# Performance work log

Hardware: AMD Instinct MI355X
Metric: run time of the kernel (lower is better)

## Reference

```python
import jax, jax.numpy as jnp
import numpy as np

B = 1
HEIGHT, WIDTH = 30, 52
HW = HEIGHT * WIDTH            # 1560
TQ = 2                         # query blocks -> Qtot = 3120
TK = 8                         # history blocks -> Ktot = 12480
KPQ = 2                        # selected kv blocks per query block
QTOT = TQ * HW
KTOT = TK * HW
HEADS = 12
DH = 128
DIM = HEADS * DH               # 1536, inner_dim == dim
EPS = 1e-5


def _rope_tables(S, D):
    # interleaved RoPE tables: freqs_cos[..., 0::2] == cos(ang), freqs_sin[..., 1::2] == sin(ang)
    inv_freq = 1.0 / (10000.0 ** (np.arange(0, D, 2, dtype=np.float32) / D))
    ang = np.arange(S, dtype=np.float32)[:, None] * inv_freq[None, :]      # [S, D/2]
    cos = np.repeat(np.cos(ang), 2, axis=-1)                                # [S, D]
    sin = np.repeat(np.sin(ang), 2, axis=-1)
    return (jnp.asarray(cos)[None, :, None, :], jnp.asarray(sin)[None, :, None, :])


def setup_inputs() -> dict:
    key = jax.random.key(0)
    ks = jax.random.split(key, 12)
    hidden_states = jax.random.normal(ks[0], (B, QTOT, DIM), jnp.float32)
    history_states = jax.random.normal(ks[1], (B, KTOT, DIM), jnp.float32)
    freqs_cos, freqs_sin = _rope_tables(QTOT, DH)
    freqs_cos_his, freqs_sin_his = _rope_tables(KTOT, DH)
    # first selected block always valid, second may be -1 (masked)
    sel0 = jax.random.randint(ks[2], (B, TQ, 1), 0, TK)
    sel1 = jax.random.randint(ks[3], (B, TQ, 1), -1, TK)
    sel_k_blocks = jnp.concatenate([sel0, sel1], axis=-1).astype(jnp.int32)  # [B, TQ, KPQ]
    s = 0.02
    Wq = jax.random.normal(ks[4], (DIM, DIM), jnp.float32) * s
    Wk = jax.random.normal(ks[5], (DIM, DIM), jnp.float32) * s
    Wv = jax.random.normal(ks[6], (DIM, DIM), jnp.float32) * s
    Wo = jax.random.normal(ks[7], (DIM, DIM), jnp.float32) * s
    bq = jnp.zeros((DIM,), jnp.float32)
    bk = jnp.zeros((DIM,), jnp.float32)
    bv = jnp.zeros((DIM,), jnp.float32)
    bo = jnp.zeros((DIM,), jnp.float32)
    gq = jnp.ones((DIM,), jnp.float32)
    gk = jnp.ones((DIM,), jnp.float32)
    return dict(hidden_states=hidden_states, history_states=history_states,
                freqs_cos=freqs_cos, freqs_sin=freqs_sin,
                freqs_cos_his=freqs_cos_his, freqs_sin_his=freqs_sin_his,
                sel_k_blocks=sel_k_blocks,
                Wq=Wq, bq=bq, Wk=Wk, bk=bk, Wv=Wv, bv=bv, Wo=Wo, bo=bo, gq=gq, gk=gk)


def _rmsnorm(x, g):
    return x * jax.lax.rsqrt(jnp.mean(x * x, axis=-1, keepdims=True) + EPS) * g


def _apply_rope(x, fc, fs):
    # x: [B, S, H, D]; fc/fs: [1, S, 1, D] interleaved tables
    x1 = x[..., 0::2]
    x2 = x[..., 1::2]
    cos = fc[..., 0::2]
    sin = fs[..., 1::2]
    even = x1 * cos - x2 * sin
    odd = x1 * sin + x2 * cos
    return jnp.stack([even, odd], axis=-1).reshape(x.shape)


def reference(hidden_states, history_states, freqs_cos, freqs_sin,
              freqs_cos_his, freqs_sin_his, sel_k_blocks,
              Wq, bq, Wk, bk, Wv, bv, Wo, bo, gq, gk):
    Bn, Qtot, _ = hidden_states.shape
    # projections + RMSNorm
    q = _rmsnorm(hidden_states @ Wq.T + bq, gq)
    k = _rmsnorm(history_states @ Wk.T + bk, gk)
    v = history_states @ Wv.T + bv
    q = q.reshape(Bn, QTOT, HEADS, DH)
    k = k.reshape(Bn, KTOT, HEADS, DH)
    v = v.reshape(Bn, KTOT, HEADS, DH)
    q = _apply_rope(q, freqs_cos, freqs_sin)
    k = _apply_rope(k, freqs_cos_his, freqs_sin_his)
    # [B, Hh, S, D] then blocked
    q_blk = q.transpose(0, 2, 1, 3).reshape(Bn, HEADS, TQ, HW, DH)
    k_blk = k.transpose(0, 2, 1, 3).reshape(Bn, HEADS, TK, HW, DH)
    v_blk = v.transpose(0, 2, 1, 3).reshape(Bn, HEADS, TK, HW, DH)
    # gather selected kv blocks (clamped indices; invalid masked later)
    idx = jnp.clip(sel_k_blocks, 0).reshape(Bn, TQ * KPQ)          # [B, TQ*KPQ]
    gather = jax.vmap(lambda kb, ib: kb[:, ib])                     # over batch
    k_sel = gather(k_blk, idx).reshape(Bn, HEADS, TQ, KPQ * HW, DH)
    v_sel = gather(v_blk, idx).reshape(Bn, HEADS, TQ, KPQ * HW, DH)
    scale = 1.0 / jnp.sqrt(jnp.float32(DH))
    scores = jnp.einsum('bhtqd,bhtkd->bhtqk', q_blk, k_sel) * scale  # [B,Hh,TQ,HW,KPQ*HW]
    valid = (sel_k_blocks >= 0)                                      # [B,TQ,KPQ]
    mask = jnp.repeat(valid, HW, axis=-1)[:, None, :, None, :]       # [B,1,TQ,1,KPQ*HW]
    scores = jnp.where(mask, scores, -jnp.inf)
    attnw = jax.nn.softmax(scores, axis=-1)
    out = jnp.einsum('bhtqk,bhtkd->bhtqd', attnw, v_sel)             # [B,Hh,TQ,HW,DH]
    out = out.reshape(Bn, HEADS, QTOT, DH).transpose(0, 2, 1, 3).reshape(Bn, QTOT, HEADS * DH)
    return out @ Wo.T + bo
```

## Files before the change

kernel.cpp:

```cpp
#include <hip/hip_runtime.h>

typedef unsigned short u16;
typedef __attribute__((ext_vector_type(4))) unsigned short u16x4;
typedef __attribute__((ext_vector_type(8))) unsigned short u16x8;
typedef __attribute__((ext_vector_type(4))) short s16x4;
typedef __attribute__((ext_vector_type(4))) float f32x4;
typedef __attribute__((ext_vector_type(8))) __bf16 bf16x8;

__device__ __forceinline__ u16 f2bf(float f) {
  union { float f; unsigned int u; } v; v.f = f;
  unsigned int u = v.u;
  unsigned int r = (u + 0x7fffu + ((u >> 16) & 1u)) >> 16;
  return (u16)r;
}
__device__ __forceinline__ u16 f2bf_hw(float f) {
  return __builtin_bit_cast(u16, (__bf16)f);
}
__device__ __forceinline__ float bf2f(u16 h) {
  union { unsigned int u; float f; } v; v.u = ((unsigned int)h) << 16;
  return v.f;
}
__device__ __forceinline__ f32x4 mfma16(u16x8 a, u16x8 b, f32x4 c) {
  return __builtin_amdgcn_mfma_f32_16x16x32_bf16(
      __builtin_bit_cast(bf16x8, a), __builtin_bit_cast(bf16x8, b), c, 0, 0, 0);
}
__device__ __forceinline__ f32x4 mfma16k16(u16x4 a, u16x4 b, f32x4 c) {
  return __builtin_amdgcn_mfma_f32_16x16x16bf16_1k(
      __builtin_bit_cast(s16x4, a), __builtin_bit_cast(s16x4, b), c, 0, 0, 0);
}
__device__ __forceinline__ void glds16(const void* g, void* l) {
  __builtin_amdgcn_global_load_lds((const __attribute__((address_space(1))) void*)g,
                                   (__attribute__((address_space(3))) void*)l, 16, 0, 0);
}
__device__ __forceinline__ int xcd_chunk(int bid, int nwg) {
  int xcd = bid & 7, idx = bid >> 3;
  int q = nwg >> 3, r = nwg & 7;
  int base = xcd < r ? xcd * (q + 1) : r * (q + 1) + (xcd - r) * q;
  return base + idx;
}
__device__ __forceinline__ int sel_mask(const int* __restrict__ sel) {
  int m = 0;
#pragma unroll
  for (int tt = 0; tt < 2; ++tt) {
    int a = sel[2 * tt];
    if (a < 0) a = 0;
    m |= 1 << a;
    int b = sel[2 * tt + 1];
    if (b >= 0) m |= 1 << b;
  }
  return m;
}

__global__ __launch_bounds__(256) void cvt_all(
    const float* __restrict__ hs, const float* __restrict__ his,
    const float* __restrict__ Wq, const float* __restrict__ Wk,
    const float* __restrict__ Wv, const float* __restrict__ Wo,
    u16* __restrict__ hsb, u16* __restrict__ hib,
    u16* __restrict__ wqb, u16* __restrict__ wkb,
    u16* __restrict__ wvb, u16* __restrict__ wob) {
  const int N0 = 1198080, N1 = 5990400, N2 = 6580224, N3 = 7170048, N4 = 7759872;
  int i = blockIdx.x * 256 + threadIdx.x;
  const float* s; u16* o; int base;
  if (i < N0)      { s = hs;  o = hsb; base = 0;  }
  else if (i < N1) { s = his; o = hib; base = N0; }
  else if (i < N2) { s = Wq;  o = wqb; base = N1; }
  else if (i < N3) { s = Wk;  o = wkb; base = N2; }
  else if (i < N4) { s = Wv;  o = wvb; base = N3; }
  else             { s = Wo;  o = wob; base = N4; }
  int j = i - base;
  float4 v = ((const float4*)s)[j];
  u16x4 r;
  r.x = f2bf(v.x); r.y = f2bf(v.y); r.z = f2bf(v.z); r.w = f2bf(v.w);
  ((u16x4*)o)[j] = r;
}

template <int OUT, int NBX>
__global__ __launch_bounds__(256, 2) void gemm_v2(
    const u16* __restrict__ A, const u16* __restrict__ W,
    const float* __restrict__ bias, void* __restrict__ Cp, int M) {
  const int K = 1536, N = 1536;
  __shared__ __align__(16) u16 gsm[17408];
  u16* As = gsm;
  u16* Bs = gsm + 8192;
  const int tid = threadIdx.x;
  const int lane = tid & 63, wid = tid >> 6;
  const int quad = lane >> 4, l15 = lane & 15;
  const int lg = xcd_chunk(blockIdx.x, gridDim.x);
  const int m0 = (lg / NBX) * 128, n0 = (lg % NBX) * 128;
  const int wm = (wid >> 1) * 64, wn = (wid & 1) * 64;
  f32x4 acc[4][4];
#pragma unroll
  for (int i = 0; i < 4; ++i)
#pragma unroll
    for (int j = 0; j < 4; ++j)
#pragma unroll
      for (int r = 0; r < 4; ++r) acc[i][j][r] = 0.f;

  const int r8 = lane >> 3, c8 = lane & 7;
  const int gch = c8 ^ r8;

  for (int k0 = 0; k0 < K; k0 += 64) {
#pragma unroll
    for (int inst = 0; inst < 4; ++inst) {
      int row = wid * 32 + inst * 8 + r8;
      glds16(A + ((size_t)(m0 + row) * K + k0 + gch * 8), As + (wid * 32 + inst * 8) * 64);
      glds16(W + ((size_t)(n0 + row) * K + k0 + gch * 8), Bs + (wid * 32 + inst * 8) * 64);
    }
    asm volatile("s_waitcnt vmcnt(0)" ::: "memory");
    __syncthreads();
#pragma unroll
    for (int ks = 0; ks < 2; ++ks) {
      u16x8 af[4], bfr[4];
#pragma unroll
      for (int i = 0; i < 4; ++i) {
        int row = wm + i * 16 + l15;
        af[i] = *(const u16x8*)&As[row * 64 + (((ks * 4 + quad) ^ (l15 & 7)) * 8)];
      }
#pragma unroll
      for (int j = 0; j < 4; ++j) {
        int row = wn + j * 16 + l15;
        bfr[j] = *(const u16x8*)&Bs[row * 64 + (((ks * 4 + quad) ^ (l15 & 7)) * 8)];
      }
#pragma unroll
      for (int i = 0; i < 4; ++i)
#pragma unroll
        for (int j = 0; j < 4; ++j) acc[i][j] = mfma16(af[i], bfr[j], acc[i][j]);
    }
    __syncthreads();
  }

#pragma unroll
  for (int i = 0; i < 4; ++i) {
    int row = m0 + wm + i * 16 + quad * 4;
#pragma unroll
    for (int j = 0; j < 4; ++j) {
      int col = n0 + wn + j * 16 + l15;
      float bc = bias[col];
#pragma unroll
      for (int r = 0; r < 4; ++r) {
        if (row + r < M) {
          float v = acc[i][j][r] + bc;
          if (OUT == 1)
            ((float*)Cp)[(size_t)(row + r) * N + col] = v;
          else
            ((u16*)Cp)[(size_t)(row + r) * N + col] = f2bf(v);
        }
      }
    }
  }
}

__global__ __launch_bounds__(256, 2) void gemm_kv(
    const u16* __restrict__ A, const u16* __restrict__ Wkv,
    const float* __restrict__ bk, const float* __restrict__ bv,
    u16* __restrict__ Ck, u16* __restrict__ Vt,
    const int* __restrict__ sel, int M, int ldt) {
  const int K = 1536;
  __shared__ __align__(16) u16 gsm[17408];
  u16* As = gsm;
  u16* Bs = gsm + 8192;
  const int tid = threadIdx.x;
  const int lane = tid & 63, wid = tid >> 6;
  const int quad = lane >> 4, l15 = lane & 15;
  const int lg = xcd_chunk(blockIdx.x, gridDim.x);
  const int qtr = lg / 588;
  const int rem = lg % 588;
  const int mi = rem / 6;
  const int m0 = ((mi * 25) % 98) * 128;
  const int n0 = (qtr * 6 + rem % 6) * 128;

  {
    int mask = sel_mask(sel);
    int tb0 = m0 / 1560;
    int tb1 = (m0 + 127) / 1560;
    if (!((mask >> tb0) & 1) && !((mask >> tb1) & 1)) return;
  }

  const int wm = (wid >> 1) * 64, wn = (wid & 1) * 64;
  f32x4 acc[4][4];
#pragma unroll
  for (int i = 0; i < 4; ++i)
#pragma unroll
    for (int j = 0; j < 4; ++j)
#pragma unroll
      for (int r = 0; r < 4; ++r) acc[i][j][r] = 0.f;

  const int r8 = lane >> 3, c8 = lane & 7;
  const int gch = c8 ^ r8;

  for (int k0 = 0; k0 < K; k0 += 64) {
#pragma unroll
    for (int inst = 0; inst < 4; ++inst) {
      int row = wid * 32 + inst * 8 + r8;
      glds16(A + ((size_t)(m0 + row) * K + k0 + gch * 8), As + (wid * 32 + inst * 8) * 64);
      glds16(Wkv + ((size_t)(n0 + row) * K + k0 + gch * 8), Bs + (wid * 32 + inst * 8) * 64);
    }
    asm volatile("s_waitcnt vmcnt(0)" ::: "memory");
    __syncthreads();
#pragma unroll
    for (int ks = 0; ks < 2; ++ks) {
      u16x8 af[4], bfr[4];
#pragma unroll
      for (int i = 0; i < 4; ++i) {
        int row = wm + i * 16 + l15;
        af[i] = *(const u16x8*)&As[row * 64 + (((ks * 4 + quad) ^ (l15 & 7)) * 8)];
      }
#pragma unroll
      for (int j = 0; j < 4; ++j) {
        int row = wn + j * 16 + l15;
        bfr[j] = *(const u16x8*)&Bs[row * 64 + (((ks * 4 + quad) ^ (l15 & 7)) * 8)];
      }
#pragma unroll
      for (int i = 0; i < 4; ++i)
#pragma unroll
        for (int j = 0; j < 4; ++j) acc[i][j] = mfma16(af[i], bfr[j], acc[i][j]);
    }
    __syncthreads();
  }

  if (n0 < 1536) {
#pragma unroll
    for (int i = 0; i < 4; ++i) {
      int row = m0 + wm + i * 16 + quad * 4;
#pragma unroll
      for (int j = 0; j < 4; ++j) {
        int col = n0 + wn + j * 16 + l15;
        float bc = bk[col];
#pragma unroll
        for (int r = 0; r < 4; ++r) {
          if (row + r < M)
            Ck[(size_t)(row + r) * 1536 + col] = f2bf(acc[i][j][r] + bc);
        }
      }
    }
  } else {
    const int n0v = n0 - 1536;
    u16* Ct = gsm;
#pragma unroll
    for (int i = 0; i < 4; ++i)
#pragma unroll
      for (int j = 0; j < 4; ++j) {
        int nloc = wn + j * 16 + l15;
        float bc = bv[n0v + nloc];
#pragma unroll
        for (int r = 0; r < 4; ++r) {
          int mloc = wm + i * 16 + quad * 4 + r;
          Ct[nloc * 136 + mloc] = f2bf(acc[i][j][r] + bc);
        }
      }
    __syncthreads();
    int n = tid >> 1, half = tid & 1;
#pragma unroll
    for (int e = 0; e < 8; ++e) {
      int mloc = half * 64 + e * 8;
      if (m0 + mloc < M) {
        u16x8 v = *(const u16x8*)&Ct[n * 136 + mloc];
        *(u16x8*)(Vt + (size_t)(n0v + n) * ldt + m0 + mloc) = v;
      }
    }
  }
}

__global__ __launch_bounds__(192) void norm_rope2(u16* __restrict__ X,
                                                  const float* __restrict__ g,
                                                  const float* __restrict__ fc,
                                                  const float* __restrict__ fs,
                                                  float oscale,
                                                  const int* __restrict__ sel) {
  const int DIMc = 1536;
  int row = blockIdx.x;
  if (sel) {
    int mask = sel_mask(sel);
    if (!((mask >> (row / 1560)) & 1)) return;
  }
  int tid = threadIdx.x;
  u16* xr = X + (size_t)row * DIMc + tid * 8;
  u16x8 v = *(const u16x8*)xr;
  float x[8];
  float ss = 0.f;
#pragma unroll
  for (int e = 0; e < 8; ++e) { x[e] = bf2f(v[e]); ss += x[e] * x[e]; }
#pragma unroll
  for (int m = 1; m < 64; m <<= 1) ss += __shfl_xor(ss, m);
  __shared__ float w3[3];
  if ((tid & 63) == 0) w3[tid >> 6] = ss;
  __syncthreads();
  float rs = rsqrtf((w3[0] + w3[1] + w3[2]) * (1.f / 1536.f) + 1e-5f);
  int dhb = (tid * 8) & 127;
  const float* fcr = fc + (size_t)row * 128 + dhb;
  const float* fsr = fs + (size_t)row * 128 + dhb;
  float4 c0 = *(const float4*)fcr, c1 = *(const float4*)(fcr + 4);
  float4 s0 = *(const float4*)fsr, s1 = *(const float4*)(fsr + 4);
  const float* gp = g + tid * 8;
  float4 g0 = *(const float4*)gp, g1 = *(const float4*)(gp + 4);
  float cosv[4] = {c0.x, c0.z, c1.x, c1.z};
  float sinv[4] = {s0.y, s0.w, s1.y, s1.w};
  float gv[8] = {g0.x, g0.y, g0.z, g0.w, g1.x, g1.y, g1.z, g1.w};
  u16x8 o;
#pragma unroll
  for (int p = 0; p < 4; ++p) {
    float a = x[2 * p] * rs * gv[2 * p];
    float b = x[2 * p + 1] * rs * gv[2 * p + 1];
    o[2 * p] = f2bf((a * cosv[p] - b * sinv[p]) * oscale);
    o[2 * p + 1] = f2bf((a * sinv[p] + b * cosv[p]) * oscale);
  }
  *(u16x8*)xr = o;
}

__global__ __launch_bounds__(256, 3) void attn12(
    const u16* __restrict__ Q, const u16* __restrict__ Kb,
    const u16* __restrict__ VT, const int* __restrict__ sel,
    float* __restrict__ Oacc, float* __restrict__ Lp) {
  const int HWc = 1560, DIMc = 1536, KTt = 12480, NT = 600;
  __shared__ __align__(16) u16 smem[16384];
  const int tid = threadIdx.x;
  const int lane = tid & 63, wid = tid >> 6;
  const int quad = lane >> 4, l15 = lane & 15;

  int bid = blockIdx.x;
  int xcd = bid & 7, idx = bid >> 3;
  int mt = idx / 12, il = idx % 12;
  int u = xcd + 8 * (il >> 1);
  const int t = il & 1;
  const int seg = u / 12;
  const int h = u % 12;
  const int m0 = mt * 128;
  const int g = h * 2 + t;

  int s0v = sel[2 * t];
  const int b0 = s0v > 0 ? s0v : 0;
  const int b1 = sel[2 * t + 1];
  const int nk = (b1 >= 0) ? 2 * HWc : HWc;
  const int nch = (nk + 31) >> 5;
  const int cpseg = (nch + 3) >> 2;
  const int c0 = seg * cpseg;
  const int c1 = (c0 + cpseg < nch) ? c0 + cpseg : nch;

  u16x8 qf[2][4];
#pragma unroll
  for (int qt = 0; qt < 2; ++qt) {
    int qrow = m0 + wid * 32 + qt * 16 + l15;
    if (qrow > HWc - 1) qrow = HWc - 1;
    const u16* qp = Q + (size_t)(t * HWc + qrow) * DIMc + h * 128;
#pragma unroll
    for (int ks = 0; ks < 4; ++ks) qf[qt][ks] = *(const u16x8*)(qp + ks * 32 + quad * 8);
  }

  f32x4 oacc[2][8];
#pragma unroll
  for (int qt = 0; qt < 2; ++qt)
#pragma unroll
    for (int m = 0; m < 8; ++m)
#pragma unroll
      for (int r = 0; r < 4; ++r) oacc[qt][m][r] = 0.f;
  float lp[2] = {0.f, 0.f};

  auto stage = [&](int kc, int buf) {
    u16* Ks = smem + buf * 4096;
    u16* Vt = smem + 8192 + buf * 4096;
#pragma unroll
    for (int n = 0; n < 2; ++n) {
      int kl = wid * 8 + n * 4 + (lane >> 4);
      int gc = (lane & 15) ^ (kl & 15);
      int kg = kc + kl;
      if (kg >= nk) kg = 0;
      int big = kg >= HWc;
      int tok = (big ? b1 : b0) * HWc + kg - (big ? HWc : 0);
      glds16(Kb + ((size_t)tok * DIMc + h * 128 + gc * 8), Ks + (wid * 8 + n * 4) * 128);
    }
#pragma unroll
    for (int n = 0; n < 2; ++n) {
      int dl = wid * 32 + n * 16 + (lane >> 2);
      int gc = (lane & 3) ^ (dl & 3) ^ ((dl >> 2) & 3);
      int tg = kc + gc * 8;
      if (tg >= nk) tg = 0;
      int big = tg >= HWc;
      int tok = (big ? b1 : b0) * HWc + tg - (big ? HWc : 0);
      glds16(VT + ((size_t)(h * 128 + dl) * KTt + tok), Vt + (wid * 32 + n * 16) * 32);
    }
  };

  if (c0 < c1) stage(c0 * 32, 0);

  for (int c = c0; c < c1; ++c) {
    const int buf = (c - c0) & 1;
    u16* Ks = smem + buf * 4096;
    u16* Vt = smem + 8192 + buf * 4096;
    asm volatile("s_waitcnt vmcnt(0)\n\ts_barrier" ::: "memory");
    if (c + 1 < c1) stage((c + 1) * 32, buf ^ 1);

    f32x4 s[2][2];
#pragma unroll
    for (int gg = 0; gg < 2; ++gg)
#pragma unroll
      for (int qt = 0; qt < 2; ++qt)
#pragma unroll
        for (int r = 0; r < 4; ++r) s[gg][qt][r] = 0.f;
#pragma unroll
    for (int ks = 0; ks < 4; ++ks)
#pragma unroll
      for (int gg = 0; gg < 2; ++gg) {
        u16x8 ka = *(const u16x8*)&Ks[(gg * 16 + l15) * 128 + (((ks * 4 + quad) ^ l15) * 8)];
#pragma unroll
        for (int qt = 0; qt < 2; ++qt) s[gg][qt] = mfma16(ka, qf[qt][ks], s[gg][qt]);
      }

    float p[2][2][4];
#pragma unroll
    for (int gg = 0; gg < 2; ++gg)
#pragma unroll
      for (int qt = 0; qt < 2; ++qt)
#pragma unroll
        for (int r = 0; r < 4; ++r) p[gg][qt][r] = exp2f(s[gg][qt][r]);
    if ((c + 1) * 32 > nk) {
#pragma unroll
      for (int gg = 0; gg < 2; ++gg)
#pragma unroll
        for (int r = 0; r < 4; ++r) {
          bool bad = c * 32 + gg * 16 + quad * 4 + r >= nk;
          if (bad) {
#pragma unroll
            for (int qt = 0; qt < 2; ++qt) p[gg][qt][r] = 0.f;
          }
        }
    }
    u16x4 pb[2][2];
#pragma unroll
    for (int gg = 0; gg < 2; ++gg)
#pragma unroll
      for (int qt = 0; qt < 2; ++qt)
#pragma unroll
        for (int r = 0; r < 4; ++r) {
          lp[qt] += p[gg][qt][r];
          pb[gg][qt][r] = f2bf_hw(p[gg][qt][r]);
        }

#pragma unroll
    for (int m = 0; m < 8; ++m) {
      int d = m * 16 + l15;
#pragma unroll
      for (int gg = 0; gg < 2; ++gg) {
        int sl = (gg * 2 + (quad >> 1)) ^ (d & 3) ^ ((d >> 2) & 3);
        u16x4 va = *(const u16x4*)&Vt[d * 32 + sl * 8 + (quad & 1) * 4];
#pragma unroll
        for (int qt = 0; qt < 2; ++qt) oacc[qt][m] = mfma16k16(va, pb[gg][qt], oacc[qt][m]);
      }
    }
  }

#pragma unroll
  for (int qt = 0; qt < 2; ++qt) {
    lp[qt] += __shfl_xor(lp[qt], 16);
    lp[qt] += __shfl_xor(lp[qt], 32);
  }
#pragma unroll
  for (int qt = 0; qt < 2; ++qt) {
    int qrow0 = m0 + wid * 32 + qt * 16;
    if (qrow0 < HWc) {
      size_t sb = ((size_t)seg * NT + g * 25 + (qrow0 >> 6)) * 64 + (qrow0 & 63);
      if (lane < 16 && qrow0 + lane < HWc) Lp[sb + lane] = lp[qt];
      if (qrow0 + l15 < HWc) {
#pragma unroll
        for (int m = 0; m < 8; ++m)
          *(f32x4*)&Oacc[(sb + l15) * 128 + m * 16 + quad * 4] = oacc[qt][m];
      }
    }
  }
}

__global__ __launch_bounds__(256) void attn_norm(const float* __restrict__ Oacc,
                                                 const float* __restrict__ Lp,
                                                 u16* __restrict__ O) {
  const int HWc = 1560, DIMc = 1536, NT = 600;
  int tile = blockIdx.x;
  int g = tile / 25, mt = tile % 25;
  int h = g >> 1, t = g & 1;
  int m0 = mt * 64;
  int tid = threadIdx.x;
#pragma unroll
  for (int e = 0; e < 8; ++e) {
    int idx = e * 256 + tid;
    int qloc = idx >> 5;
    int d4 = (idx & 31) * 4;
    int q = m0 + qloc;
    if (q < HWc) {
      f32x4 a = {0.f, 0.f, 0.f, 0.f};
      float l = 0.f;
#pragma unroll
      for (int s = 0; s < 4; ++s) {
        const size_t sbase = ((size_t)s * NT + tile) * 64 + qloc;
        f32x4 v = *(const f32x4*)&Oacc[sbase * 128 + d4];
#pragma unroll
        for (int r = 0; r < 4; ++r) a[r] += v[r];
        l += Lp[sbase];
      }
      float linv = 1.f / l;
      u16x4 o;
#pragma unroll
      for (int r = 0; r < 4; ++r) o[r] = f2bf(a[r] * linv);
      *(u16x4*)(O + (size_t)(t * HWc + q) * DIMc + h * 128 + d4) = o;
    }
  }
}

extern "C" void kernel_launch(void* const* d_in, const int* in_sizes, int n_in,
                              void* d_out, int out_size, void* d_ws, size_t ws_size,
                              hipStream_t stream) {
  const float* hs  = (const float*)d_in[0];
  const float* his = (const float*)d_in[1];
  const float* fc  = (const float*)d_in[2];
  const float* fs  = (const float*)d_in[3];
  const float* fch = (const float*)d_in[4];
  const float* fsh = (const float*)d_in[5];
  const int*   sel = (const int*)d_in[6];
  const float* Wq  = (const float*)d_in[7];
  const float* bq  = (const float*)d_in[8];
  const float* Wk  = (const float*)d_in[9];
  const float* bk  = (const float*)d_in[10];
  const float* Wv  = (const float*)d_in[11];
  const float* bv  = (const float*)d_in[12];
  const float* Wo  = (const float*)d_in[13];
  const float* bo  = (const float*)d_in[14];
  const float* gq  = (const float*)d_in[15];
  const float* gk  = (const float*)d_in[16];

  const int QT = 3120, KT = 12480, DIMc = 1536;
  u16* p = (u16*)d_ws;
  u16* qb  = p; p += (size_t)QT * DIMc;
  u16* kb2 = p; p += (size_t)KT * DIMc;
  u16* vt  = p; p += (size_t)DIMc * KT;
  u16* ab  = p; p += (size_t)QT * DIMc;
  u16* wob = p; p += (size_t)DIMc * DIMc;
  u16* scratch = p;
  u16* hsb = scratch;
  u16* hib = hsb + (size_t)QT * DIMc;
  u16* wqb = hib + (size_t)KT * DIMc;
  u16* wkb = wqb + (size_t)DIMc * DIMc;
  u16* wvb = wkb + (size_t)DIMc * DIMc;
  float* oaccb = (float*)scratch;
  float* lpb   = oaccb + (size_t)4 * 600 * 64 * 128;

  cvt_all<<<dim3(32616), 256, 0, stream>>>(hs, his, Wq, Wk, Wv, Wo,
                                           hsb, hib, wqb, wkb, wvb, wob);

  gemm_v2<0, 12><<<dim3(300), 256, 0, stream>>>(hsb, wqb, bq, qb, QT);
  gemm_kv<<<dim3(2352), 256, 0, stream>>>(hib, wkb, bk, bv, kb2, vt, sel, KT, KT);

  const float qscale = (float)(0.08838834764831845 * 1.4426950408889634);
  norm_rope2<<<dim3(QT), 192, 0, stream>>>(qb, gq, fc, fs, qscale, nullptr);
  norm_rope2<<<dim3(KT), 192, 0, stream>>>(kb2, gk, fch, fsh, 1.0f, sel);

  attn12<<<dim3(1248), 256, 0, stream>>>(qb, kb2, vt, sel, oaccb, lpb);
  attn_norm<<<dim3(600), 256, 0, stream>>>(oaccb, lpb, ab);

  gemm_v2<1, 12><<<dim3(300), 256, 0, stream>>>(ab, wob, bo, d_out, QT);
}
```

Measured before the change: 471.5 us.

## Balance attention split-K segments across query blocks by selected KV length

The attention kernel used to give each (head, query block) a fixed 4 KV segments, even when one query block has only one valid KV block and so half the work. It now hands 6 segment slots per head to the two query blocks in proportion to their chunk counts, which shrinks the grid from 1248 to 936 workgroups and evens out per-workgroup work. The normalisation kernel reads the same selection to know how many partial segments to sum. The segment count is now data-dependent and relies on the hardcoded 98/49 chunk counts.

```diff
diff --git a/kernel.cpp b/kernel.cpp
--- a/kernel.cpp
+++ b/kernel.cpp
@@ -307,7 +307,7 @@
   *(u16x8*)xr = o;
 }
 
-__global__ __launch_bounds__(256, 3) void attn12(
+__global__ __launch_bounds__(256, 3) void attn13(
     const u16* __restrict__ Q, const u16* __restrict__ Kb,
     const u16* __restrict__ VT, const int* __restrict__ sel,
     float* __restrict__ Oacc, float* __restrict__ Lp) {
@@ -319,11 +319,17 @@
 
   int bid = blockIdx.x;
   int xcd = bid & 7, idx = bid >> 3;
-  int mt = idx / 12, il = idx % 12;
-  int u = xcd + 8 * (il >> 1);
-  const int t = il & 1;
-  const int seg = u / 12;
-  const int h = u % 12;
+  int ug = idx / 13, mt = idx % 13;
+  int u = xcd + 8 * ug;
+  const int h = u / 6;
+  const int slot = u % 6;
+
+  const int nch0 = (sel[1] >= 0) ? 98 : 49;
+  const int nch1 = (sel[3] >= 0) ? 98 : 49;
+  const int ns0 = 6 * nch0 / (nch0 + nch1);
+  const int t = (slot < ns0) ? 0 : 1;
+  const int si = (slot < ns0) ? slot : slot - ns0;
+  const int nseg = (slot < ns0) ? ns0 : 6 - ns0;
   const int m0 = mt * 128;
   const int g = h * 2 + t;
 
@@ -331,9 +337,9 @@
   const int b0 = s0v > 0 ? s0v : 0;
   const int b1 = sel[2 * t + 1];
   const int nk = (b1 >= 0) ? 2 * HWc : HWc;
-  const int nch = (nk + 31) >> 5;
-  const int cpseg = (nch + 3) >> 2;
-  const int c0 = seg * cpseg;
+  const int nch = (b1 >= 0) ? 98 : 49;
+  const int cpseg = (nch + nseg - 1) / nseg;
+  const int c0 = si * cpseg;
   const int c1 = (c0 + cpseg < nch) ? c0 + cpseg : nch;
 
   u16x8 qf[2][4];
@@ -457,7 +463,7 @@
   for (int qt = 0; qt < 2; ++qt) {
     int qrow0 = m0 + wid * 32 + qt * 16;
     if (qrow0 < HWc) {
-      size_t sb = ((size_t)seg * NT + g * 25 + (qrow0 >> 6)) * 64 + (qrow0 & 63);
+      size_t sb = ((size_t)si * NT + g * 25 + (qrow0 >> 6)) * 64 + (qrow0 & 63);
       if (lane < 16 && qrow0 + lane < HWc) Lp[sb + lane] = lp[qt];
       if (qrow0 + l15 < HWc) {
 #pragma unroll
@@ -470,6 +476,7 @@
 
 __global__ __launch_bounds__(256) void attn_norm(const float* __restrict__ Oacc,
                                                  const float* __restrict__ Lp,
+                                                 const int* __restrict__ sel,
                                                  u16* __restrict__ O) {
   const int HWc = 1560, DIMc = 1536, NT = 600;
   int tile = blockIdx.x;
@@ -477,6 +484,10 @@
   int h = g >> 1, t = g & 1;
   int m0 = mt * 64;
   int tid = threadIdx.x;
+  const int nch0 = (sel[1] >= 0) ? 98 : 49;
+  const int nch1 = (sel[3] >= 0) ? 98 : 49;
+  const int ns0 = 6 * nch0 / (nch0 + nch1);
+  const int nseg = (t == 0) ? ns0 : 6 - ns0;
 #pragma unroll
   for (int e = 0; e < 8; ++e) {
     int idx = e * 256 + tid;
@@ -486,8 +497,7 @@
     if (q < HWc) {
       f32x4 a = {0.f, 0.f, 0.f, 0.f};
       float l = 0.f;
-#pragma unroll
-      for (int s = 0; s < 4; ++s) {
+      for (int s = 0; s < nseg; ++s) {
         const size_t sbase = ((size_t)s * NT + tile) * 64 + qloc;
         f32x4 v = *(const f32x4*)&Oacc[sbase * 128 + d4];
 #pragma unroll
@@ -550,8 +560,8 @@
   norm_rope2<<<dim3(QT), 192, 0, stream>>>(qb, gq, fc, fs, qscale, nullptr);
   norm_rope2<<<dim3(KT), 192, 0, stream>>>(kb2, gk, fch, fsh, 1.0f, sel);
 
-  attn12<<<dim3(1248), 256, 0, stream>>>(qb, kb2, vt, sel, oaccb, lpb);
-  attn_norm<<<dim3(600), 256, 0, stream>>>(oaccb, lpb, ab);
+  attn13<<<dim3(936), 256, 0, stream>>>(qb, kb2, vt, sel, oaccb, lpb);
+  attn_norm<<<dim3(600), 256, 0, stream>>>(oaccb, lpb, sel, ab);
 
   gemm_v2<1, 12><<<dim3(300), 256, 0, stream>>>(ab, wob, bo, d_out, QT);
 }
```

After: 460.2 us. 2.4% less time.
